# Optimization experiments

Hardware: AMD Instinct MI355X
Metric: run time of the kernel (lower is better)

The kernel has to match this reference:

```python
import jax, jax.numpy as jnp
import numpy as np

NUM_HEADS = 12
HEAD_DIM = 32
GP_NUM = 20


def setup_inputs() -> dict:
    key = jax.random.key(0)
    k1, k2, k3, k4 = jax.random.split(key, 4)
    B, H, W, C = 4, 32, 32, 384
    att = NUM_HEADS * HEAD_DIM  # == C (required by single group_mode)
    x = jax.random.normal(k1, (B, H, W, C), dtype=jnp.float32)
    W_qkv = jax.random.normal(k2, (3 * att, C), dtype=jnp.float32) * (C ** -0.5)
    W_proj = jax.random.normal(k3, (C, att), dtype=jnp.float32) * (att ** -0.5)
    W_gp = jax.random.normal(k4, (GP_NUM, C), dtype=jnp.float32) * (C ** -0.5)
    return {"x": x, "W_qkv": W_qkv, "W_proj": W_proj, "W_gp": W_gp}


def reference(x, W_qkv, W_proj, W_gp):
    B, H, W_, C = x.shape
    N = H * W_
    h, d = NUM_HEADS, HEAD_DIM
    scale = d ** -0.5

    qkv = x.reshape(B, N, C) @ W_qkv.T                      # [B,N,3hd]
    q, k, v = jnp.split(qkv, 3, axis=-1)
    q = q.reshape(B, N, h, d).transpose(0, 2, 1, 3)          # [B,h,N,d]
    k = k.reshape(B, N, h, d).transpose(0, 2, 1, 3)
    v = v.reshape(B, N, h, d).transpose(0, 2, 1, 3)

    attn = jax.nn.softmax(jnp.einsum('bhnd,bhmd->bhnm', q, k) * scale, axis=-1)

    # single group mode: hard top-1 group assignment from all-head q
    q_all = q.transpose(0, 2, 1, 3).reshape(B, N, h * d)     # [B,N,hd]
    gw = q_all @ W_gp.T                                      # [B,N,GP_NUM]
    oh = jax.nn.one_hot(jnp.argmax(gw, axis=-1), GP_NUM, dtype=attn.dtype)
    G = jnp.einsum('bng,bmg->bnm', oh, oh)                   # [B,N,N] same-group mask
    Gh = jnp.concatenate([
        jnp.broadcast_to(G[:, None], (B, h // 2, N, N)),
        jnp.broadcast_to(1.0 - G[:, None], (B, h // 2, N, N)),
    ], axis=1)                                               # [B,h,N,N]

    attn = attn * Gh
    # unusual column-wise renorm: sum over query axis (dim=2)
    attn = attn / (attn.sum(axis=2, keepdims=True) + 1e-8)

    out = jnp.einsum('bhnm,bhmd->bhnd', attn, v)
    out = out.transpose(0, 2, 1, 3).reshape(B, H, W_, h * d)
    return out @ W_proj.T
```

## Files before the change

### kernel.cpp

```cpp
#include <hip/hip_runtime.h>
#include <hip/hip_bf16.h>


#define B_    4
#define N_    1024
#define C_    384
#define H3_   1152
#define NH_   12
#define HD_   32
#define GP_   20
#define BH_   48
#define SCALE 0.17677669529663687f

typedef __attribute__((ext_vector_type(8))) short bf16x8;
typedef __attribute__((ext_vector_type(4))) float f32x4;

static __device__ __forceinline__ unsigned short f2bf(float x) {
  union { float f; unsigned u; } v; v.f = x;
  unsigned r = v.u + 0x7fff + ((v.u >> 16) & 1);
  return (unsigned short)(r >> 16);
}
static __device__ __forceinline__ float bf2f(unsigned short h) {
  union { unsigned u; float f; } v; v.u = ((unsigned)h) << 16;
  return v.f;
}

__global__ __launch_bounds__(256) void conv3(const float* __restrict__ x,
                                             const float* __restrict__ wq,
                                             const float* __restrict__ wp,
                                             unsigned short* __restrict__ xh,
                                             unsigned short* __restrict__ xl,
                                             unsigned short* __restrict__ wqh,
                                             unsigned short* __restrict__ wql,
                                             unsigned short* __restrict__ wph,
                                             unsigned short* __restrict__ wpl) {
  const int NX = (4096 * C_) / 4, NQ = (H3_ * C_) / 4, NP = (C_ * C_) / 4;
  int idx = blockIdx.x * 256 + threadIdx.x;
  const float* src; unsigned short *dh, *dl; int o;
  if (idx < NX)            { src = x;  dh = xh;  dl = xl;  o = idx; }
  else if (idx < NX + NQ)  { src = wq; dh = wqh; dl = wql; o = idx - NX; }
  else if (idx < NX + NQ + NP) { src = wp; dh = wph; dl = wpl; o = idx - NX - NQ; }
  else return;
  float4 v = *(const float4*)(src + (size_t)o * 4);
  float a[4] = {v.x, v.y, v.z, v.w};
  unsigned short h[4], lo[4];
  #pragma unroll
  for (int i = 0; i < 4; ++i) { h[i] = f2bf(a[i]); lo[i] = f2bf(a[i] - bf2f(h[i])); }
  uint2 ph = {(unsigned)h[0]  | ((unsigned)h[1]  << 16),
              (unsigned)h[2]  | ((unsigned)h[3]  << 16)};
  uint2 pl = {(unsigned)lo[0] | ((unsigned)lo[1] << 16),
              (unsigned)lo[2] | ((unsigned)lo[3] << 16)};
  *(uint2*)(dh + (size_t)o * 4) = ph;
  *(uint2*)(dl + (size_t)o * 4) = pl;
}

__global__ __launch_bounds__(256) void wgp_fuse(const float* __restrict__ Wqkv,
                                                const float* __restrict__ Wgp,
                                                double* __restrict__ M) {
  int idx = blockIdx.x * 256 + threadIdx.x;
  if (idx >= GP_ * C_) return;
  int g = idx / C_, c = idx % C_;
  double acc = 0.0;
  for (int j = 0; j < C_; ++j)
    acc += (double)Wgp[g * C_ + j] * (double)Wqkv[(size_t)j * C_ + c];
  M[idx] = acc;
}

__global__ __launch_bounds__(320) void group_assign2(const float* __restrict__ x,
                                                     const double* __restrict__ M,
                                                     int* __restrict__ group) {
  __shared__ double sc[16][GP_];
  int tid = threadIdx.x;
  int r = tid / GP_, g = tid % GP_;
  int n = blockIdx.x * 16 + r;
  const float* row = x + (size_t)n * C_;
  const double* w = M + (size_t)g * C_;
  double acc = 0.0;
  for (int c = 0; c < C_; ++c) acc += (double)row[c] * w[c];
  sc[r][g] = acc;
  __syncthreads();
  if (g == 0) {
    int best = 0; double bv = sc[r][0];
    #pragma unroll
    for (int j = 1; j < GP_; ++j)
      if (sc[r][j] > bv) { bv = sc[r][j]; best = j; }
    group[n] = best;
  }
}

__global__ __launch_bounds__(256) void gemm_qkv(
    const unsigned short* __restrict__ Ah_g, const unsigned short* __restrict__ Al_g,
    const unsigned short* __restrict__ Bh_g, const unsigned short* __restrict__ Bl_g,
    unsigned short* __restrict__ Qh, unsigned short* __restrict__ Ql,
    unsigned short* __restrict__ Kh, unsigned short* __restrict__ Kl,
    float* __restrict__ Vf) {
  __shared__ __align__(16) unsigned short sAh[128 * 32];
  __shared__ __align__(16) unsigned short sAl[128 * 32];
  __shared__ __align__(16) unsigned short sBh[128 * 32];
  __shared__ __align__(16) unsigned short sBl[128 * 32];
  int tid = threadIdx.x;
  int l = tid & 63, w = tid >> 6;
  int lanelo = l & 15, g16 = l >> 4;
  int wr = w >> 1, wc = w & 1;
  int bn = blockIdx.x, bm = blockIdx.y;

  const unsigned short* sg;
  unsigned short* sd;
  int rb;
  if (w == 0)      { sg = Ah_g; sd = sAh; rb = bm; }
  else if (w == 1) { sg = Al_g; sd = sAl; rb = bm; }
  else if (w == 2) { sg = Bh_g; sd = sBh; rb = bn; }
  else             { sg = Bl_g; sd = sBl; rb = bn; }
  int srow = l >> 2, sc4 = l & 3;
  const unsigned short* gsrc = sg + (size_t)(rb * 128 + srow) * C_ + sc4 * 8;
  unsigned short* ldst = sd + srow * 32 + ((sc4 ^ (srow & 3)) * 8);

  f32x4 acc[4][4];
  #pragma unroll
  for (int i = 0; i < 4; ++i)
    #pragma unroll
    for (int j = 0; j < 4; ++j) acc[i][j] = (f32x4){0.f, 0.f, 0.f, 0.f};

  for (int kk = 0; kk < 12; ++kk) {
    if (kk) __syncthreads();
    #pragma unroll
    for (int i = 0; i < 8; ++i)
      *(uint4*)(ldst + i * 16 * 32) =
          *(const uint4*)(gsrc + (size_t)(i * 16) * C_ + kk * 32);
    __syncthreads();
    bf16x8 ah[4], al[4], bh8[4], bl8[4];
    #pragma unroll
    for (int i = 0; i < 4; ++i) {
      int row = wr * 64 + i * 16 + lanelo;
      int off = row * 32 + ((g16 ^ (row & 3)) * 8);
      ah[i] = *(const bf16x8*)(sAh + off);
      al[i] = *(const bf16x8*)(sAl + off);
    }
    #pragma unroll
    for (int j = 0; j < 4; ++j) {
      int row = wc * 64 + j * 16 + lanelo;
      int off = row * 32 + ((g16 ^ (row & 3)) * 8);
      bh8[j] = *(const bf16x8*)(sBh + off);
      bl8[j] = *(const bf16x8*)(sBl + off);
    }
    #pragma unroll
    for (int i = 0; i < 4; ++i)
      #pragma unroll
      for (int j = 0; j < 4; ++j) {
        acc[i][j] = __builtin_amdgcn_mfma_f32_16x16x32_bf16(ah[i], bh8[j], acc[i][j], 0, 0, 0);
        acc[i][j] = __builtin_amdgcn_mfma_f32_16x16x32_bf16(ah[i], bl8[j], acc[i][j], 0, 0, 0);
        acc[i][j] = __builtin_amdgcn_mfma_f32_16x16x32_bf16(al[i], bh8[j], acc[i][j], 0, 0, 0);
      }
  }

  int region = bn / 3;
  #pragma unroll
  for (int i = 0; i < 4; ++i) {
    int mm0 = bm * 128 + wr * 64 + i * 16 + g16 * 4;
    #pragma unroll
    for (int j = 0; j < 4; ++j) {
      int c = bn * 128 + wc * 64 + j * 16 + lanelo;
      int cc = c - region * 384;
      #pragma unroll
      for (int t = 0; t < 4; ++t) {
        int mm = mm0 + t;
        int b = mm >> 10, n = mm & 1023;
        float v = acc[i][j][t];
        if (region == 0) {
          v *= SCALE;
          unsigned short h = f2bf(v), lo = f2bf(v - bf2f(h));
          size_t idx = ((size_t)(b * NH_ + (cc >> 5)) * N_ + n) * HD_ + (cc & 31);
          Qh[idx] = h; Ql[idx] = lo;
        } else if (region == 1) {
          unsigned short h = f2bf(v), lo = f2bf(v - bf2f(h));
          size_t idx = ((size_t)(b * NH_ + (cc >> 5)) * N_ + n) * HD_ + (cc & 31);
          Kh[idx] = h; Kl[idx] = lo;
        } else {
          Vf[(size_t)mm * C_ + cc] = v;
        }
      }
    }
  }
}

__global__ __launch_bounds__(256) void gemm_proj(
    const unsigned short* __restrict__ Ah_g, const unsigned short* __restrict__ Al_g,
    const unsigned short* __restrict__ Bh_g, const unsigned short* __restrict__ Bl_g,
    float* __restrict__ Cm) {
  __shared__ __align__(16) unsigned short sAh[64 * 32];
  __shared__ __align__(16) unsigned short sAl[64 * 32];
  __shared__ __align__(16) unsigned short sBh[64 * 32];
  __shared__ __align__(16) unsigned short sBl[64 * 32];
  int tid = threadIdx.x;
  int l = tid & 63, w = tid >> 6;
  int lanelo = l & 15, g16 = l >> 4;
  int wr = w >> 1, wc = w & 1;
  int bn = blockIdx.x, bm = blockIdx.y;

  int srow = tid >> 2, sc4 = tid & 3;
  size_t aoff = (size_t)(bm * 64 + srow) * C_ + sc4 * 8;
  size_t boff = (size_t)(bn * 64 + srow) * C_ + sc4 * 8;
  int ldoff = srow * 32 + ((sc4 ^ (srow & 3)) * 8);

  f32x4 acc[2][2];
  #pragma unroll
  for (int i = 0; i < 2; ++i)
    #pragma unroll
    for (int j = 0; j < 2; ++j) acc[i][j] = (f32x4){0.f, 0.f, 0.f, 0.f};

  for (int kk = 0; kk < 12; ++kk) {
    if (kk) __syncthreads();
    *(uint4*)(sAh + ldoff) = *(const uint4*)(Ah_g + aoff + kk * 32);
    *(uint4*)(sAl + ldoff) = *(const uint4*)(Al_g + aoff + kk * 32);
    *(uint4*)(sBh + ldoff) = *(const uint4*)(Bh_g + boff + kk * 32);
    *(uint4*)(sBl + ldoff) = *(const uint4*)(Bl_g + boff + kk * 32);
    __syncthreads();
    bf16x8 ah[2], al[2], bh8[2], bl8[2];
    #pragma unroll
    for (int i = 0; i < 2; ++i) {
      int row = wr * 32 + i * 16 + lanelo;
      int off = row * 32 + ((g16 ^ (row & 3)) * 8);
      ah[i] = *(const bf16x8*)(sAh + off);
      al[i] = *(const bf16x8*)(sAl + off);
    }
    #pragma unroll
    for (int j = 0; j < 2; ++j) {
      int row = wc * 32 + j * 16 + lanelo;
      int off = row * 32 + ((g16 ^ (row & 3)) * 8);
      bh8[j] = *(const bf16x8*)(sBh + off);
      bl8[j] = *(const bf16x8*)(sBl + off);
    }
    #pragma unroll
    for (int i = 0; i < 2; ++i)
      #pragma unroll
      for (int j = 0; j < 2; ++j) {
        acc[i][j] = __builtin_amdgcn_mfma_f32_16x16x32_bf16(ah[i], bh8[j], acc[i][j], 0, 0, 0);
        acc[i][j] = __builtin_amdgcn_mfma_f32_16x16x32_bf16(ah[i], bl8[j], acc[i][j], 0, 0, 0);
        acc[i][j] = __builtin_amdgcn_mfma_f32_16x16x32_bf16(al[i], bh8[j], acc[i][j], 0, 0, 0);
      }
  }
  #pragma unroll
  for (int i = 0; i < 2; ++i) {
    int mm = bm * 64 + wr * 32 + i * 16 + g16 * 4;
    #pragma unroll
    for (int j = 0; j < 2; ++j) {
      int c = bn * 64 + wc * 32 + j * 16 + lanelo;
      #pragma unroll
      for (int t = 0; t < 4; ++t)
        Cm[(size_t)(mm + t) * C_ + c] = acc[i][j][t];
    }
  }
}

__global__ __launch_bounds__(256) void score3(const unsigned short* __restrict__ Qh,
                                              const unsigned short* __restrict__ Ql,
                                              const unsigned short* __restrict__ Kh,
                                              const unsigned short* __restrict__ Kl,
                                              const int* __restrict__ group,
                                              float* __restrict__ rinv,
                                              float* __restrict__ colpart) {
  __shared__ __align__(16) unsigned short kbufh[4096];
  __shared__ __align__(16) unsigned short kbufl[4096];
  __shared__ float colpart_s[4][1024];
  __shared__ int g_s[1024];
  int tid = threadIdx.x;
  int l = tid & 63, w = tid >> 6;
  int lanelo = l & 15, g16 = l >> 4;
  int flat = blockIdx.y * 16 + blockIdx.x;
  int nf = (flat & 7) * 96 + (flat >> 3);
  int bh = nf >> 4, blk = nf & 15;
  int b = bh / NH_;
  bool samehead = ((bh % NH_) < NH_ / 2);
  int q0 = blk * 64 + w * 16;
  size_t bhb = (size_t)bh * (N_ * HD_);

  *(int4*)&g_s[tid * 4] = *(const int4*)(group + b * N_ + tid * 4);
  bf16x8 aQh = *(const bf16x8*)(Qh + bhb + (size_t)(q0 + lanelo) * HD_ + g16 * 8);
  bf16x8 aQl = *(const bf16x8*)(Ql + bhb + (size_t)(q0 + lanelo) * HD_ + g16 * 8);
  __syncthreads();
  int gq[4];
  #pragma unroll
  for (int t = 0; t < 4; ++t) gq[t] = g_s[q0 + g16 * 4 + t];

  float s4[4] = {0.f, 0.f, 0.f, 0.f};
  for (int ch = 0; ch < 8; ++ch) {
    __syncthreads();
    #pragma unroll
    for (int t2 = 0; t2 < 2; ++t2) {
      int f2 = t2 * 256 + tid;
      int row = f2 >> 2, c4 = f2 & 3;
      uint4 vh = *(const uint4*)(Kh + bhb + (size_t)(ch * 128 + row) * HD_ + c4 * 8);
      uint4 vl = *(const uint4*)(Kl + bhb + (size_t)(ch * 128 + row) * HD_ + c4 * 8);
      int phys = row * 64 + ((c4 ^ (row & 3)) << 4);
      *(uint4*)((char*)kbufh + phys) = vh;
      *(uint4*)((char*)kbufl + phys) = vl;
    }
    __syncthreads();
    #pragma unroll
    for (int kt2 = 0; kt2 < 8; ++kt2) {
      int kvl = kt2 * 16 + lanelo;
      int phys = kvl * 64 + ((g16 ^ (kvl & 3)) << 4);
      bf16x8 bh8 = *(const bf16x8*)((char*)kbufh + phys);
      bf16x8 bl8 = *(const bf16x8*)((char*)kbufl + phys);
      f32x4 acc = {0.f, 0.f, 0.f, 0.f};
      acc = __builtin_amdgcn_mfma_f32_16x16x32_bf16(aQh, bh8, acc, 0, 0, 0);
      acc = __builtin_amdgcn_mfma_f32_16x16x32_bf16(aQh, bl8, acc, 0, 0, 0);
      acc = __builtin_amdgcn_mfma_f32_16x16x32_bf16(aQl, bh8, acc, 0, 0, 0);
      #pragma unroll
      for (int t = 0; t < 4; ++t) s4[t] += __expf(acc[t]);
    }
  }
  float ri[4];
  #pragma unroll
  for (int t = 0; t < 4; ++t) {
    #pragma unroll
    for (int off = 1; off < 16; off <<= 1) s4[t] += __shfl_xor(s4[t], off);
    ri[t] = 1.0f / s4[t];
  }
  if (lanelo == 0) {
    #pragma unroll
    for (int t = 0; t < 4; ++t)
      rinv[(size_t)bh * N_ + q0 + g16 * 4 + t] = ri[t];
  }

  for (int ch = 0; ch < 8; ++ch) {
    __syncthreads();
    #pragma unroll
    for (int t2 = 0; t2 < 2; ++t2) {
      int f2 = t2 * 256 + tid;
      int row = f2 >> 2, c4 = f2 & 3;
      uint4 vh = *(const uint4*)(Kh + bhb + (size_t)(ch * 128 + row) * HD_ + c4 * 8);
      uint4 vl = *(const uint4*)(Kl + bhb + (size_t)(ch * 128 + row) * HD_ + c4 * 8);
      int phys = row * 64 + ((c4 ^ (row & 3)) << 4);
      *(uint4*)((char*)kbufh + phys) = vh;
      *(uint4*)((char*)kbufl + phys) = vl;
    }
    __syncthreads();
    #pragma unroll
    for (int kt2 = 0; kt2 < 8; ++kt2) {
      int kt = ch * 8 + kt2;
      int kvl = kt2 * 16 + lanelo;
      int phys = kvl * 64 + ((g16 ^ (kvl & 3)) << 4);
      bf16x8 bh8 = *(const bf16x8*)((char*)kbufh + phys);
      bf16x8 bl8 = *(const bf16x8*)((char*)kbufl + phys);
      f32x4 acc = {0.f, 0.f, 0.f, 0.f};
      acc = __builtin_amdgcn_mfma_f32_16x16x32_bf16(aQh, bh8, acc, 0, 0, 0);
      acc = __builtin_amdgcn_mfma_f32_16x16x32_bf16(aQh, bl8, acc, 0, 0, 0);
      acc = __builtin_amdgcn_mfma_f32_16x16x32_bf16(aQl, bh8, acc, 0, 0, 0);
      int gcol = g_s[kt * 16 + lanelo];
      float cs = 0.f;
      #pragma unroll
      for (int t = 0; t < 4; ++t) {
        bool keep = ((gcol == gq[t]) == samehead);
        cs += keep ? __expf(acc[t]) * ri[t] : 0.f;
      }
      cs += __shfl_xor(cs, 16);
      cs += __shfl_xor(cs, 32);
      if (l < 16) colpart_s[w][kt * 16 + l] = cs;
    }
  }
  __syncthreads();
  int c0 = tid * 4;
  float4 p0 = *(float4*)&colpart_s[0][c0];
  float4 p1 = *(float4*)&colpart_s[1][c0];
  float4 p2 = *(float4*)&colpart_s[2][c0];
  float4 p3 = *(float4*)&colpart_s[3][c0];
  float4 rr = {p0.x + p1.x + p2.x + p3.x, p0.y + p1.y + p2.y + p3.y,
               p0.z + p1.z + p2.z + p3.z, p0.w + p1.w + p2.w + p3.w};
  *(float4*)(colpart + ((size_t)(bh * 16 + blk)) * 1024 + c0) = rr;
}

__global__ __launch_bounds__(256) void vsplit(const float* __restrict__ colpart,
                                              const float* __restrict__ Vf,
                                              unsigned short* __restrict__ Vth,
                                              unsigned short* __restrict__ Vtl) {
  __shared__ float red[256];
  __shared__ float colinv_s[16];
  __shared__ unsigned short vh_s[32][16];
  __shared__ unsigned short vl_s[32][16];
  int tid = threadIdx.x;
  int flat = blockIdx.y * 64 + blockIdx.x;
  int nf = (flat & 7) * 384 + (flat >> 3);
  int bh = nf >> 6, mt = nf & 63;
  int b = bh / NH_, hd = bh % NH_;

  int p = tid >> 4, m16 = tid & 15;
  red[tid] = colpart[((size_t)(bh * 16 + p)) * 1024 + mt * 16 + m16];
  __syncthreads();
  #pragma unroll
  for (int st = 128; st >= 16; st >>= 1) {
    if (tid < st) red[tid] += red[tid + st];
    __syncthreads();
  }
  if (tid < 16) colinv_s[tid] = 1.0f / (red[tid] + 1e-8f);
  __syncthreads();
  if (tid < 128) {
    int m = tid >> 3, d4 = (tid & 7) * 4;
    float4 v = *(const float4*)(Vf + ((size_t)(b * N_ + mt * 16 + m)) * C_ +
                                hd * HD_ + d4);
    float ci = colinv_s[m];
    float va[4] = {v.x * ci, v.y * ci, v.z * ci, v.w * ci};
    #pragma unroll
    for (int i = 0; i < 4; ++i) {
      unsigned short h = f2bf(va[i]);
      vh_s[d4 + i][m] = h;
      vl_s[d4 + i][m] = f2bf(va[i] - bf2f(h));
    }
  }
  __syncthreads();
  if (tid < 64) {
    int d = tid >> 1, m8 = (tid & 1) * 8;
    uint4 h = *(uint4*)&vh_s[d][m8];
    *(uint4*)(Vth + ((size_t)bh * HD_ + d) * N_ + mt * 16 + m8) = h;
  } else if (tid < 128) {
    int t2 = tid - 64;
    int d = t2 >> 1, m8 = (t2 & 1) * 8;
    uint4 lo = *(uint4*)&vl_s[d][m8];
    *(uint4*)(Vtl + ((size_t)bh * HD_ + d) * N_ + mt * 16 + m8) = lo;
  }
}

__global__ __launch_bounds__(256) void pv3(const unsigned short* __restrict__ Qh,
                                           const unsigned short* __restrict__ Ql,
                                           const unsigned short* __restrict__ Kh,
                                           const unsigned short* __restrict__ Kl,
                                           const unsigned short* __restrict__ Vth,
                                           const unsigned short* __restrict__ Vtl,
                                           const int* __restrict__ group,
                                           const float* __restrict__ rinv,
                                           unsigned short* __restrict__ aoh,
                                           unsigned short* __restrict__ aol) {
  __shared__ __align__(16) unsigned short kbufh[4096];
  __shared__ __align__(16) unsigned short kbufl[4096];
  __shared__ __align__(16) unsigned short vbufh[4096];
  __shared__ __align__(16) unsigned short vbufl[4096];
  __shared__ __align__(16) float bounce[4][512];
  __shared__ int g_s[1024];
  int tid = threadIdx.x;
  int l = tid & 63, w = tid >> 6;
  int lanelo = l & 15, g16 = l >> 4;
  int flat = blockIdx.y * 16 + blockIdx.x;
  int nf = (flat & 7) * 96 + (flat >> 3);
  int bh = nf >> 4, blk = nf & 15;
  int b = bh / NH_, hd = bh % NH_;
  bool samehead = (hd < NH_ / 2);
  int q0 = blk * 64 + w * 16;
  size_t bhb = (size_t)bh * (N_ * HD_);

  *(int4*)&g_s[tid * 4] = *(const int4*)(group + b * N_ + tid * 4);
  bf16x8 aQh = *(const bf16x8*)(Qh + bhb + (size_t)(q0 + lanelo) * HD_ + g16 * 8);
  bf16x8 aQl = *(const bf16x8*)(Ql + bhb + (size_t)(q0 + lanelo) * HD_ + g16 * 8);
  float ri[4];
  #pragma unroll
  for (int t = 0; t < 4; ++t)
    ri[t] = rinv[(size_t)bh * N_ + q0 + g16 * 4 + t];
  __syncthreads();
  int gq[4];
  #pragma unroll
  for (int t = 0; t < 4; ++t) gq[t] = g_s[q0 + g16 * 4 + t];

  f32x4 o0 = {0.f, 0.f, 0.f, 0.f};
  f32x4 o1 = {0.f, 0.f, 0.f, 0.f};

  for (int ch = 0; ch < 8; ++ch) {
    __syncthreads();
    #pragma unroll
    for (int t2 = 0; t2 < 2; ++t2) {
      int f2 = t2 * 256 + tid;
      int row = f2 >> 2, c4 = f2 & 3;
      uint4 vh = *(const uint4*)(Kh + bhb + (size_t)(ch * 128 + row) * HD_ + c4 * 8);
      uint4 vl = *(const uint4*)(Kl + bhb + (size_t)(ch * 128 + row) * HD_ + c4 * 8);
      int phys = row * 64 + ((c4 ^ (row & 3)) << 4);
      *(uint4*)((char*)kbufh + phys) = vh;
      *(uint4*)((char*)kbufl + phys) = vl;
    }
    #pragma unroll
    for (int t2 = 0; t2 < 2; ++t2) {
      int f2 = t2 * 256 + tid;
      int d = f2 >> 4, c = f2 & 15;
      uint4 vh = *(const uint4*)(Vth + bhb + (size_t)d * N_ + ch * 128 + c * 8);
      uint4 vl = *(const uint4*)(Vtl + bhb + (size_t)d * N_ + ch * 128 + c * 8);
      int physc = c ^ (d & 15);
      *(uint4*)(vbufh + d * 128 + physc * 8) = vh;
      *(uint4*)(vbufl + d * 128 + physc * 8) = vl;
    }
    __syncthreads();

    #pragma unroll
    for (int pair = 0; pair < 4; ++pair) {
      f32x4 sa[2];
      #pragma unroll
      for (int half = 0; half < 2; ++half) {
        int kvl = pair * 32 + half * 16 + lanelo;
        int phys = kvl * 64 + ((g16 ^ (kvl & 3)) << 4);
        bf16x8 bh8 = *(const bf16x8*)((char*)kbufh + phys);
        bf16x8 bl8 = *(const bf16x8*)((char*)kbufl + phys);
        f32x4 acc = {0.f, 0.f, 0.f, 0.f};
        acc = __builtin_amdgcn_mfma_f32_16x16x32_bf16(aQh, bh8, acc, 0, 0, 0);
        acc = __builtin_amdgcn_mfma_f32_16x16x32_bf16(aQh, bl8, acc, 0, 0, 0);
        acc = __builtin_amdgcn_mfma_f32_16x16x32_bf16(aQl, bh8, acc, 0, 0, 0);
        sa[half] = acc;
      }
      #pragma unroll
      for (int half = 0; half < 2; ++half) {
        int kvloc = pair * 32 + half * 16 + lanelo;
        int gcol = g_s[ch * 128 + kvloc];
        int kv = half * 16 + lanelo;
        int chunk = kv >> 2;
        #pragma unroll
        for (int t = 0; t < 4; ++t) {
          bool keep = ((gcol == gq[t]) == samehead);
          float p = keep ? __expf(sa[half][t]) : 0.f;
          int q = g16 * 4 + t;
          bounce[w][q * 32 + ((chunk ^ (q & 7)) << 2) + (kv & 3)] = p;
        }
      }
      float pf[8];
      int q2 = lanelo;
      int c0i = (2 * g16) ^ (q2 & 7), c1i = (2 * g16 + 1) ^ (q2 & 7);
      *(float4*)&pf[0] = *(float4*)&bounce[w][q2 * 32 + c0i * 4];
      *(float4*)&pf[4] = *(float4*)&bounce[w][q2 * 32 + c1i * 4];
      bf16x8 pa;
      #pragma unroll
      for (int j = 0; j < 8; ++j) pa[j] = (short)f2bf(pf[j]);
      int vchunk = pair * 4 + g16;
      int d0 = lanelo, d1 = 16 + lanelo;
      bf16x8 v0h = *(const bf16x8*)(vbufh + d0 * 128 + ((vchunk ^ (d0 & 15)) << 3));
      bf16x8 v0l = *(const bf16x8*)(vbufl + d0 * 128 + ((vchunk ^ (d0 & 15)) << 3));
      bf16x8 v1h = *(const bf16x8*)(vbufh + d1 * 128 + ((vchunk ^ (d1 & 15)) << 3));
      bf16x8 v1l = *(const bf16x8*)(vbufl + d1 * 128 + ((vchunk ^ (d1 & 15)) << 3));
      o0 = __builtin_amdgcn_mfma_f32_16x16x32_bf16(pa, v0h, o0, 0, 0, 0);
      o0 = __builtin_amdgcn_mfma_f32_16x16x32_bf16(pa, v0l, o0, 0, 0, 0);
      o1 = __builtin_amdgcn_mfma_f32_16x16x32_bf16(pa, v1h, o1, 0, 0, 0);
      o1 = __builtin_amdgcn_mfma_f32_16x16x32_bf16(pa, v1l, o1, 0, 0, 0);
    }
  }
  #pragma unroll
  for (int t = 0; t < 4; ++t) {
    size_t row = (size_t)(b * N_ + q0 + g16 * 4 + t) * C_ + hd * HD_;
    float v0 = o0[t] * ri[t], v1 = o1[t] * ri[t];
    unsigned short h;
    h = f2bf(v0); aoh[row + lanelo]      = h; aol[row + lanelo]      = f2bf(v0 - bf2f(h));
    h = f2bf(v1); aoh[row + 16 + lanelo] = h; aol[row + 16 + lanelo] = f2bf(v1 - bf2f(h));
  }
}

extern "C" void kernel_launch(void* const* d_in, const int* in_sizes, int n_in,
                              void* d_out, int out_size, void* d_ws, size_t ws_size,
                              hipStream_t stream) {
  const float* x     = (const float*)d_in[0];
  const float* Wqkv  = (const float*)d_in[1];
  const float* Wproj = (const float*)d_in[2];
  const float* Wgp   = (const float*)d_in[3];
  float* out = (float*)d_out;

  char* base = (char*)d_ws;
  size_t off = 0;
  auto alloc = [&](size_t bytes) {
    void* p = base + off;
    off += (bytes + 255) & ~(size_t)255;
    return p;
  };
  float*  Vf      = (float*)alloc(4096ull * C_ * 4);
  float*  rinv    = (float*)alloc((size_t)BH_ * N_ * 4);
  float*  colpart = (float*)alloc((size_t)BH_ * 16 * N_ * 4);
  double* Mgp     = (double*)alloc((size_t)GP_ * C_ * 8);
  int*    group   = (int*)alloc(4096ull * 4);
  unsigned short* xh  = (unsigned short*)alloc(4096ull * C_ * 2);
  unsigned short* xl  = (unsigned short*)alloc(4096ull * C_ * 2);
  unsigned short* Wqh = (unsigned short*)alloc((size_t)H3_ * C_ * 2);
  unsigned short* Wql = (unsigned short*)alloc((size_t)H3_ * C_ * 2);
  unsigned short* Wph = (unsigned short*)alloc((size_t)C_ * C_ * 2);
  unsigned short* Wpl = (unsigned short*)alloc((size_t)C_ * C_ * 2);
  unsigned short* aoh = (unsigned short*)alloc(4096ull * C_ * 2);
  unsigned short* aol = (unsigned short*)alloc(4096ull * C_ * 2);
  const size_t BSZ = (size_t)BH_ * N_ * HD_;
  unsigned short* Qh  = (unsigned short*)alloc(BSZ * 2);
  unsigned short* Ql  = (unsigned short*)alloc(BSZ * 2);
  unsigned short* Kh  = (unsigned short*)alloc(BSZ * 2);
  unsigned short* Kl  = (unsigned short*)alloc(BSZ * 2);
  unsigned short* Vth = (unsigned short*)alloc(BSZ * 2);
  unsigned short* Vtl = (unsigned short*)alloc(BSZ * 2);

  conv3<<<dim3(2112), 256, 0, stream>>>(x, Wqkv, Wproj, xh, xl, Wqh, Wql, Wph, Wpl);
  wgp_fuse<<<dim3(30), 256, 0, stream>>>(Wqkv, Wgp, Mgp);
  group_assign2<<<dim3(256), 320, 0, stream>>>(x, Mgp, group);
  gemm_qkv<<<dim3(9, 32), 256, 0, stream>>>(xh, xl, Wqh, Wql,
                                            Qh, Ql, Kh, Kl, Vf);
  score3<<<dim3(16, BH_), 256, 0, stream>>>(Qh, Ql, Kh, Kl, group, rinv, colpart);
  vsplit<<<dim3(64, BH_), 256, 0, stream>>>(colpart, Vf, Vth, Vtl);
  pv3<<<dim3(16, BH_), 256, 0, stream>>>(Qh, Ql, Kh, Kl, Vth, Vtl, group,
                                         rinv, aoh, aol);
  gemm_proj<<<dim3(6, 64), 256, 0, stream>>>(aoh, aol, Wph, Wpl, out);
}
```

Before: 176.9 us.

## Double-buffer QKV and proj GEMMs with register prefetch, smaller tiles, XCD swizzle

Both GEMM kernels now use double-buffered LDS with register prefetch of the next K-slice, which removes one barrier per iteration and overlaps global loads with MFMA work. The QKV GEMM tile shrinks from 128x128 to 128x64, doubling the grid to 576 blocks for better occupancy across CUs. Both launches move to a flat 1D grid with a block-index swizzle that groups neighbouring tiles, likely to improve cache locality across XCDs. The costs are more LDS per block and less reuse per tile in the QKV GEMM.

```diff
diff --git a/kernel.cpp b/kernel.cpp
--- a/kernel.cpp
+++ b/kernel.cpp
@@ -94,72 +94,89 @@
     unsigned short* __restrict__ Qh, unsigned short* __restrict__ Ql,
     unsigned short* __restrict__ Kh, unsigned short* __restrict__ Kl,
     float* __restrict__ Vf) {
-  __shared__ __align__(16) unsigned short sAh[128 * 32];
-  __shared__ __align__(16) unsigned short sAl[128 * 32];
-  __shared__ __align__(16) unsigned short sBh[128 * 32];
-  __shared__ __align__(16) unsigned short sBl[128 * 32];
+  __shared__ __align__(16) unsigned short sAh[2][128 * 32];
+  __shared__ __align__(16) unsigned short sAl[2][128 * 32];
+  __shared__ __align__(16) unsigned short sBh[2][64 * 32];
+  __shared__ __align__(16) unsigned short sBl[2][64 * 32];
   int tid = threadIdx.x;
   int l = tid & 63, w = tid >> 6;
   int lanelo = l & 15, g16 = l >> 4;
   int wr = w >> 1, wc = w & 1;
-  int bn = blockIdx.x, bm = blockIdx.y;
-
-  const unsigned short* sg;
-  unsigned short* sd;
-  int rb;
-  if (w == 0)      { sg = Ah_g; sd = sAh; rb = bm; }
-  else if (w == 1) { sg = Al_g; sd = sAl; rb = bm; }
-  else if (w == 2) { sg = Bh_g; sd = sBh; rb = bn; }
-  else             { sg = Bl_g; sd = sBl; rb = bn; }
-  int srow = l >> 2, sc4 = l & 3;
-  const unsigned short* gsrc = sg + (size_t)(rb * 128 + srow) * C_ + sc4 * 8;
-  unsigned short* ldst = sd + srow * 32 + ((sc4 ^ (srow & 3)) * 8);
-
-  f32x4 acc[4][4];
+  int flat = blockIdx.x;
+  int swz = (flat & 7) * 72 + (flat >> 3);
+  int bm = swz / 18, bn = swz % 18;
+
+  int ra = tid >> 2, c4 = tid & 3;
+  const unsigned short* gAh0 = Ah_g + (size_t)(bm * 128 + ra) * C_ + c4 * 8;
+  const unsigned short* gAl0 = Al_g + (size_t)(bm * 128 + ra) * C_ + c4 * 8;
+  const unsigned short* gBh0 = Bh_g + (size_t)(bn * 64 + ra) * C_ + c4 * 8;
+  const unsigned short* gBl0 = Bl_g + (size_t)(bn * 64 + ra) * C_ + c4 * 8;
+  int dsa = ra * 32 + ((c4 ^ (ra & 3)) * 8);
+
+  uint4 r0 = *(const uint4*)(gAh0);
+  uint4 r1 = *(const uint4*)(gAh0 + (size_t)64 * C_);
+  uint4 r2 = *(const uint4*)(gAl0);
+  uint4 r3 = *(const uint4*)(gAl0 + (size_t)64 * C_);
+  uint4 r4 = *(const uint4*)(gBh0);
+  uint4 r5 = *(const uint4*)(gBl0);
+
+  f32x4 acc[4][2];
   #pragma unroll
   for (int i = 0; i < 4; ++i)
     #pragma unroll
-    for (int j = 0; j < 4; ++j) acc[i][j] = (f32x4){0.f, 0.f, 0.f, 0.f};
-
+    for (int j = 0; j < 2; ++j) acc[i][j] = (f32x4){0.f, 0.f, 0.f, 0.f};
+
+  int p = 0;
   for (int kk = 0; kk < 12; ++kk) {
-    if (kk) __syncthreads();
-    #pragma unroll
-    for (int i = 0; i < 8; ++i)
-      *(uint4*)(ldst + i * 16 * 32) =
-          *(const uint4*)(gsrc + (size_t)(i * 16) * C_ + kk * 32);
-    __syncthreads();
-    bf16x8 ah[4], al[4], bh8[4], bl8[4];
+    *(uint4*)(&sAh[p][dsa])           = r0;
+    *(uint4*)(&sAh[p][dsa + 64 * 32]) = r1;
+    *(uint4*)(&sAl[p][dsa])           = r2;
+    *(uint4*)(&sAl[p][dsa + 64 * 32]) = r3;
+    *(uint4*)(&sBh[p][dsa])           = r4;
+    *(uint4*)(&sBl[p][dsa])           = r5;
+    __syncthreads();
+    if (kk < 11) {
+      int ko = (kk + 1) * 32;
+      r0 = *(const uint4*)(gAh0 + ko);
+      r1 = *(const uint4*)(gAh0 + (size_t)64 * C_ + ko);
+      r2 = *(const uint4*)(gAl0 + ko);
+      r3 = *(const uint4*)(gAl0 + (size_t)64 * C_ + ko);
+      r4 = *(const uint4*)(gBh0 + ko);
+      r5 = *(const uint4*)(gBl0 + ko);
+    }
+    bf16x8 ah[4], al[4], bh8[2], bl8[2];
     #pragma unroll
     for (int i = 0; i < 4; ++i) {
       int row = wr * 64 + i * 16 + lanelo;
       int off = row * 32 + ((g16 ^ (row & 3)) * 8);
-      ah[i] = *(const bf16x8*)(sAh + off);
-      al[i] = *(const bf16x8*)(sAl + off);
-    }
-    #pragma unroll
-    for (int j = 0; j < 4; ++j) {
-      int row = wc * 64 + j * 16 + lanelo;
+      ah[i] = *(const bf16x8*)(&sAh[p][off]);
+      al[i] = *(const bf16x8*)(&sAl[p][off]);
+    }
+    #pragma unroll
+    for (int j = 0; j < 2; ++j) {
+      int row = wc * 32 + j * 16 + lanelo;
       int off = row * 32 + ((g16 ^ (row & 3)) * 8);
-      bh8[j] = *(const bf16x8*)(sBh + off);
-      bl8[j] = *(const bf16x8*)(sBl + off);
+      bh8[j] = *(const bf16x8*)(&sBh[p][off]);
+      bl8[j] = *(const bf16x8*)(&sBl[p][off]);
     }
     #pragma unroll
     for (int i = 0; i < 4; ++i)
       #pragma unroll
-      for (int j = 0; j < 4; ++j) {
+      for (int j = 0; j < 2; ++j) {
         acc[i][j] = __builtin_amdgcn_mfma_f32_16x16x32_bf16(ah[i], bh8[j], acc[i][j], 0, 0, 0);
         acc[i][j] = __builtin_amdgcn_mfma_f32_16x16x32_bf16(ah[i], bl8[j], acc[i][j], 0, 0, 0);
         acc[i][j] = __builtin_amdgcn_mfma_f32_16x16x32_bf16(al[i], bh8[j], acc[i][j], 0, 0, 0);
       }
-  }
-
-  int region = bn / 3;
+    p ^= 1;
+  }
+
+  int region = bn / 6;
   #pragma unroll
   for (int i = 0; i < 4; ++i) {
     int mm0 = bm * 128 + wr * 64 + i * 16 + g16 * 4;
     #pragma unroll
-    for (int j = 0; j < 4; ++j) {
-      int c = bn * 128 + wc * 64 + j * 16 + lanelo;
+    for (int j = 0; j < 2; ++j) {
+      int c = bn * 64 + wc * 32 + j * 16 + lanelo;
       int cc = c - region * 384;
       #pragma unroll
       for (int t = 0; t < 4; ++t) {
@@ -187,20 +204,29 @@
     const unsigned short* __restrict__ Ah_g, const unsigned short* __restrict__ Al_g,
     const unsigned short* __restrict__ Bh_g, const unsigned short* __restrict__ Bl_g,
     float* __restrict__ Cm) {
-  __shared__ __align__(16) unsigned short sAh[64 * 32];
-  __shared__ __align__(16) unsigned short sAl[64 * 32];
-  __shared__ __align__(16) unsigned short sBh[64 * 32];
-  __shared__ __align__(16) unsigned short sBl[64 * 32];
+  __shared__ __align__(16) unsigned short sAh[2][64 * 32];
+  __shared__ __align__(16) unsigned short sAl[2][64 * 32];
+  __shared__ __align__(16) unsigned short sBh[2][64 * 32];
+  __shared__ __align__(16) unsigned short sBl[2][64 * 32];
   int tid = threadIdx.x;
   int l = tid & 63, w = tid >> 6;
   int lanelo = l & 15, g16 = l >> 4;
   int wr = w >> 1, wc = w & 1;
-  int bn = blockIdx.x, bm = blockIdx.y;
-
-  int srow = tid >> 2, sc4 = tid & 3;
-  size_t aoff = (size_t)(bm * 64 + srow) * C_ + sc4 * 8;
-  size_t boff = (size_t)(bn * 64 + srow) * C_ + sc4 * 8;
-  int ldoff = srow * 32 + ((sc4 ^ (srow & 3)) * 8);
+  int flat = blockIdx.x;
+  int swz = (flat & 7) * 48 + (flat >> 3);
+  int bm = swz / 6, bn = swz % 6;
+
+  int ra = tid >> 2, c4 = tid & 3;
+  const unsigned short* gAh0 = Ah_g + (size_t)(bm * 64 + ra) * C_ + c4 * 8;
+  const unsigned short* gAl0 = Al_g + (size_t)(bm * 64 + ra) * C_ + c4 * 8;
+  const unsigned short* gBh0 = Bh_g + (size_t)(bn * 64 + ra) * C_ + c4 * 8;
+  const unsigned short* gBl0 = Bl_g + (size_t)(bn * 64 + ra) * C_ + c4 * 8;
+  int dsa = ra * 32 + ((c4 ^ (ra & 3)) * 8);
+
+  uint4 r0 = *(const uint4*)(gAh0);
+  uint4 r1 = *(const uint4*)(gAl0);
+  uint4 r2 = *(const uint4*)(gBh0);
+  uint4 r3 = *(const uint4*)(gBl0);
 
   f32x4 acc[2][2];
   #pragma unroll
@@ -208,27 +234,34 @@
     #pragma unroll
     for (int j = 0; j < 2; ++j) acc[i][j] = (f32x4){0.f, 0.f, 0.f, 0.f};
 
+  int p = 0;
   for (int kk = 0; kk < 12; ++kk) {
-    if (kk) __syncthreads();
-    *(uint4*)(sAh + ldoff) = *(const uint4*)(Ah_g + aoff + kk * 32);
-    *(uint4*)(sAl + ldoff) = *(const uint4*)(Al_g + aoff + kk * 32);
-    *(uint4*)(sBh + ldoff) = *(const uint4*)(Bh_g + boff + kk * 32);
-    *(uint4*)(sBl + ldoff) = *(const uint4*)(Bl_g + boff + kk * 32);
-    __syncthreads();
+    *(uint4*)(&sAh[p][dsa]) = r0;
+    *(uint4*)(&sAl[p][dsa]) = r1;
+    *(uint4*)(&sBh[p][dsa]) = r2;
+    *(uint4*)(&sBl[p][dsa]) = r3;
+    __syncthreads();
+    if (kk < 11) {
+      int ko = (kk + 1) * 32;
+      r0 = *(const uint4*)(gAh0 + ko);
+      r1 = *(const uint4*)(gAl0 + ko);
+      r2 = *(const uint4*)(gBh0 + ko);
+      r3 = *(const uint4*)(gBl0 + ko);
+    }
     bf16x8 ah[2], al[2], bh8[2], bl8[2];
     #pragma unroll
     for (int i = 0; i < 2; ++i) {
       int row = wr * 32 + i * 16 + lanelo;
       int off = row * 32 + ((g16 ^ (row & 3)) * 8);
-      ah[i] = *(const bf16x8*)(sAh + off);
-      al[i] = *(const bf16x8*)(sAl + off);
+      ah[i] = *(const bf16x8*)(&sAh[p][off]);
+      al[i] = *(const bf16x8*)(&sAl[p][off]);
     }
     #pragma unroll
     for (int j = 0; j < 2; ++j) {
       int row = wc * 32 + j * 16 + lanelo;
       int off = row * 32 + ((g16 ^ (row & 3)) * 8);
-      bh8[j] = *(const bf16x8*)(sBh + off);
-      bl8[j] = *(const bf16x8*)(sBl + off);
+      bh8[j] = *(const bf16x8*)(&sBh[p][off]);
+      bl8[j] = *(const bf16x8*)(&sBl[p][off]);
     }
     #pragma unroll
     for (int i = 0; i < 2; ++i)
@@ -238,6 +271,7 @@
         acc[i][j] = __builtin_amdgcn_mfma_f32_16x16x32_bf16(ah[i], bl8[j], acc[i][j], 0, 0, 0);
         acc[i][j] = __builtin_amdgcn_mfma_f32_16x16x32_bf16(al[i], bh8[j], acc[i][j], 0, 0, 0);
       }
+    p ^= 1;
   }
   #pragma unroll
   for (int i = 0; i < 2; ++i) {
@@ -585,11 +619,11 @@
   conv3<<<dim3(2112), 256, 0, stream>>>(x, Wqkv, Wproj, xh, xl, Wqh, Wql, Wph, Wpl);
   wgp_fuse<<<dim3(30), 256, 0, stream>>>(Wqkv, Wgp, Mgp);
   group_assign2<<<dim3(256), 320, 0, stream>>>(x, Mgp, group);
-  gemm_qkv<<<dim3(9, 32), 256, 0, stream>>>(xh, xl, Wqh, Wql,
-                                            Qh, Ql, Kh, Kl, Vf);
+  gemm_qkv<<<dim3(576), 256, 0, stream>>>(xh, xl, Wqh, Wql,
+                                          Qh, Ql, Kh, Kl, Vf);
   score3<<<dim3(16, BH_), 256, 0, stream>>>(Qh, Ql, Kh, Kl, group, rinv, colpart);
   vsplit<<<dim3(64, BH_), 256, 0, stream>>>(colpart, Vf, Vth, Vtl);
   pv3<<<dim3(16, BH_), 256, 0, stream>>>(Qh, Ql, Kh, Kl, Vth, Vtl, group,
                                          rinv, aoh, aol);
-  gemm_proj<<<dim3(6, 64), 256, 0, stream>>>(aoh, aol, Wph, Wpl, out);
-}
+  gemm_proj<<<dim3(384), 256, 0, stream>>>(aoh, aol, Wph, Wpl, out);
+}
```

Result: faster. 167.2 us (-5.5%).
